# Kernel tuning notes

Measured on AMD Instinct MI355X. Metric: run time of the kernel, lower is better.

Reference implementation:

```python
import jax, jax.numpy as jnp
import numpy as np
from jax import lax


def setup_inputs() -> dict:
    key = jax.random.key(0)
    k1, k2, k3 = jax.random.split(key, 3)
    H = W = 2048
    K, p = 16, 15
    x = jax.random.uniform(k1, (1, 1, H, W), dtype=jnp.float32)
    patterns = jax.random.uniform(k2, (K, p, p), dtype=jnp.float32)
    vectors = jax.random.normal(k3, (K, 2), dtype=jnp.float32)
    return {"x": x, "patterns": patterns, "vectors": vectors}


def reference(x, patterns, vectors):
    K, p, _ = patterns.shape
    img = x[0, 0]                      # [H, W]
    H, W = img.shape
    # GENEO_1: pad by p on all sides; window at (i,j) covers padded [i:i+p, j:j+p]
    padded = jnp.pad(img, p)           # [H+2p, W+2p]
    ones_k = jnp.ones((1, 1, p, p), dtype=img.dtype)
    win_sum = lax.conv_general_dilated(
        padded[None, None], ones_k, window_strides=(1, 1), padding='VALID'
    )[0, 0]                            # [H+p+1, W+p+1]
    win_sum = win_sum[:H, :W]          # windows for i in [0,H), j in [0,W)
    # out[k,i,j] = 1 - (sum(pattern_k) - win_sum)/(p*p)
    pat_sum = patterns.sum(axis=(1, 2))                     # [K]
    F_k = 1.0 - (pat_sum[:, None, None] - win_sum[None]) / (p * p)  # [K,H,W]
    # GENEO_3: gather at (i - floor(vx), j - floor(vy)), torch negative-index wrap -> mod
    off = jnp.floor(vectors).astype(jnp.int32)              # [K,2]
    ri = (jnp.arange(H)[None, :] - off[:, 0:1]) % H          # [K,H]
    rj = (jnp.arange(W)[None, :] - off[:, 1:2]) % W          # [K,W]
    gathered = F_k[jnp.arange(K)[:, None, None], ri[:, :, None], rj[:, None, :]]  # [K,H,W]
    # original divides by final loop variable k == K-1 (faithful)
    out = gathered.sum(axis=0) / (K - 1)
    return out
```

## Files before the change

kernel.cpp:

```cpp
#include <hip/hip_runtime.h>
#include <math.h>

#define H 2048
#define W 2048
#define K 16
#define P 15
#define WP 2052
#define LDSP 272

typedef float v4 __attribute__((ext_vector_type(4)));
typedef v4 uv4 __attribute__((aligned(4)));

__global__ __launch_bounds__(320) void geneo_win(
        const float* __restrict__ img,
        float* __restrict__ win,
        const float* __restrict__ patterns,
        const float* __restrict__ vectors,
        float* __restrict__ consts,
        int* __restrict__ offs) {
    __shared__ float sl[48][LDSP];
    __shared__ float psum[5];
    int t  = threadIdx.x;
    int c0 = blockIdx.x * 256;
    int r0 = blockIdx.y * 32;

    if (blockIdx.x == 0 && blockIdx.y == 0) {
        float ps = 0.f;
        for (int idx = t; idx < 900; idx += 320) {
            v4 v = *(const v4*)&patterns[idx * 4];
            ps += (v.x + v.y) + (v.z + v.w);
        }
        #pragma unroll
        for (int q = 32; q > 0; q >>= 1) ps += __shfl_down(ps, q, 64);
        if ((t & 63) == 0) psum[t >> 6] = ps;
        if (t < 2 * K) offs[t] = (int)floorf(vectors[t]);
        __syncthreads();
        if (t == 0) {
            float total = ((psum[0] + psum[1]) + (psum[2] + psum[3])) + psum[4];
            consts[0] = (16.0f - total * (1.0f / 225.0f)) * (1.0f / 15.0f);
        }
    }

    for (int idx = t; idx < 47 * 68; idx += 320) {
        int q = idx / 68;
        int c = idx - q * 68;
        int grow = r0 - 15 + q;
        int gcol = c0 - 16 + 4 * c;
        v4 v = {0.f, 0.f, 0.f, 0.f};
        if (grow >= 0 && gcol >= 0)
            v = *(const v4*)&img[grow * W + gcol];
        *(v4*)&sl[q + 1][4 * c] = v;
    }
    __syncthreads();

    if (t < LDSP) {
        float s = 0.f;
        #pragma unroll
        for (int q = 1; q <= 15; ++q) s += sl[q][t];
        #pragma unroll
        for (int ii = 0; ii < 32; ++ii) {
            float sv = s;
            s += sl[ii + 16][t] - sl[ii + 1][t];
            sl[ii][t] = sv;
        }
    }
    __syncthreads();

    if (t < 256) {
        int g  = t & 63;
        int rb = (t >> 6) * 8;
        #pragma unroll
        for (int rr = 0; rr < 8; ++rr) {
            int ii = rb + rr;
            const float* row = &sl[ii][4 * g];
            v4 V0 = *(const v4*)&row[0];
            v4 V1 = *(const v4*)&row[4];
            v4 V2 = *(const v4*)&row[8];
            v4 V3 = *(const v4*)&row[12];
            v4 V4 = *(const v4*)&row[16];
            float s0 = ((V0.y + V0.z) + (V0.w + V1.x))
                     + ((V1.y + V1.z) + (V1.w + V2.x))
                     + ((V2.y + V2.z) + (V2.w + V3.x))
                     + ((V3.y + V3.z) + V3.w);
            float s1 = s0 - V0.y + V4.x;
            float s2 = s1 - V0.z + V4.y;
            float s3 = s2 - V0.w + V4.z;
            v4 r4 = {s0, s1, s2, s3};
            int gi = r0 + ii;
            *(v4*)&win[gi * WP + c0 + 4 * g] = r4;
            if (c0 == 0 && g == 0)
                *(v4*)&win[gi * WP + 2048] = r4;
        }
    }
}

__global__ __launch_bounds__(256) void geneo_gather(
        const float* __restrict__ win,
        const float* __restrict__ consts,
        const int* __restrict__ offs,
        float* __restrict__ out) {
    __shared__ int soy[K], sox[K];
    __shared__ float sC;
    int t = threadIdx.x;
    if (t < K) { soy[t] = offs[t * 2]; sox[t] = offs[t * 2 + 1]; }
    if (t == 0) sC = consts[0];
    __syncthreads();

    int d = blockIdx.x;
    int i = ((d & 7) << 8) | (d >> 3);
    int j = 4 * t;

    const float S = 1.0f / 3375.0f;
    v4 acc0 = {0.f, 0.f, 0.f, 0.f};
    v4 acc1 = {0.f, 0.f, 0.f, 0.f};
    #pragma unroll
    for (int k = 0; k < K; ++k) {
        int ri = (i - soy[k]) & (H - 1);
        int rj = (j - sox[k]) & (W - 1);
        const float* row = &win[ri * WP];
        acc0 += *(const uv4*)&row[rj];
        acc1 += *(const uv4*)&row[rj ^ 1024];
    }
    v4 o0 = acc0 * S + sC;
    v4 o1 = acc1 * S + sC;
    __builtin_nontemporal_store(o0, (v4*)&out[i * W + j]);
    __builtin_nontemporal_store(o1, (v4*)&out[i * W + j + 1024]);
}

extern "C" void kernel_launch(void* const* d_in, const int* in_sizes, int n_in,
                              void* d_out, int out_size, void* d_ws, size_t ws_size,
                              hipStream_t stream) {
    const float* x        = (const float*)d_in[0];
    const float* patterns = (const float*)d_in[1];
    const float* vectors  = (const float*)d_in[2];
    float* out = (float*)d_out;

    float* win    = (float*)d_ws;
    float* consts = win + H * WP;
    int*   offs   = (int*)(consts + 1);

    geneo_win<<<dim3(8, 64), 320, 0, stream>>>(x, win, patterns, vectors, consts, offs);
    geneo_gather<<<2048, 256, 0, stream>>>(win, consts, offs, out);
}
```

Baseline: 89.63 us.

## Fuse window-sum and shifted gather into one kernel using LDS halo tiles

Merges the two kernels into one. Each block computes the 15x15 window sums for its 32x256 tile plus a halo of up to 8 pixels in each direction in LDS, then gathers all 16 shifted windows from LDS instead of writing and re-reading a global window-sum buffer. A slow scalar fallback handles offsets larger than the halo, and edge blocks use wraparound masking. This removes the global intermediate round trip and one launch, at the cost of more LDS use, redundant halo work and extra complexity.

```diff
diff --git a/kernel.cpp b/kernel.cpp
--- a/kernel.cpp
+++ b/kernel.cpp
@@ -4,141 +4,212 @@
 #define H 2048
 #define W 2048
 #define K 16
-#define P 15
-#define WP 2052
-#define LDSP 272
+#define SLW 292
 
 typedef float v4 __attribute__((ext_vector_type(4)));
-typedef v4 uv4 __attribute__((aligned(4)));
-
-__global__ __launch_bounds__(320) void geneo_win(
-        const float* __restrict__ img,
-        float* __restrict__ win,
-        const float* __restrict__ patterns,
-        const float* __restrict__ vectors,
-        float* __restrict__ consts,
-        int* __restrict__ offs) {
-    __shared__ float sl[48][LDSP];
-    __shared__ float psum[5];
-    int t  = threadIdx.x;
-    int c0 = blockIdx.x * 256;
-    int r0 = blockIdx.y * 32;
-
-    if (blockIdx.x == 0 && blockIdx.y == 0) {
-        float ps = 0.f;
-        for (int idx = t; idx < 900; idx += 320) {
-            v4 v = *(const v4*)&patterns[idx * 4];
-            ps += (v.x + v.y) + (v.z + v.w);
+
+template<int S>
+__device__ __forceinline__ void gstep(const float* pk, v4* acc) {
+#pragma unroll
+  for (int rr = 0; rr < 4; ++rr) {
+    v4 A = *(const v4*)(pk + rr * SLW);
+    if constexpr (S == 0) {
+      acc[rr] += A;
+    } else {
+      v4 B = *(const v4*)(pk + rr * SLW + 4);
+      v4 r;
+      if constexpr (S == 1)      r = (v4){A.y, A.z, A.w, B.x};
+      else if constexpr (S == 2) r = (v4){A.z, A.w, B.x, B.y};
+      else                       r = (v4){A.w, B.x, B.y, B.z};
+      acc[rr] += r;
+    }
+  }
+}
+
+__global__ __launch_bounds__(512, 4) void geneo_fused(
+    const float* __restrict__ img,
+    const float* __restrict__ patterns,
+    const float* __restrict__ vectors,
+    float* __restrict__ out) {
+  __shared__ float sl[48][SLW];
+  __shared__ int   skoff[K], ssel[K], soy[K], sox[K];
+  __shared__ float sred[8];
+  __shared__ float sC;
+  __shared__ int   sfit;
+
+  const int t = threadIdx.x;
+  const int d  = blockIdx.x;
+  const int by = ((d & 7) << 3) | ((d >> 3) >> 3);
+  const int bx = (d >> 3) & 7;
+  const int i0 = by << 5;
+  const int c0 = bx << 8;
+
+  int okbit = 1;
+  if (t < K) {
+    int oy = (int)floorf(vectors[2 * t]);
+    int ox = (int)floorf(vectors[2 * t + 1]);
+    int my = oy & (H - 1); if (my > 1024) my -= 2048;
+    int mx = ox & (W - 1); if (mx > 1024) mx -= 2048;
+    soy[t] = my; sox[t] = mx;
+    int bk = 24 - mx;
+    skoff[t] = (8 - my) * SLW + (bk & ~3);
+    ssel[t]  = bk & 3;
+    okbit = (my >= -8 && my <= 8 && mx >= -8 && mx <= 8);
+  }
+  if (t < 64) {
+    unsigned long long bal = __ballot(okbit);
+    if (t == 0) sfit = ((bal & 0xFFFFull) == 0xFFFFull) ? 1 : 0;
+  }
+  float ps;
+  {
+    const v4* p4 = (const v4*)patterns;
+    v4 a = p4[t];
+    ps = (a.x + a.y) + (a.z + a.w);
+    int t2 = t + 512;
+    if (t2 < 900) { v4 b = p4[t2]; ps += (b.x + b.y) + (b.z + b.w); }
+  }
+#pragma unroll
+  for (int q2 = 32; q2 > 0; q2 >>= 1) ps += __shfl_down(ps, q2, 64);
+  if ((t & 63) == 0) sred[t >> 6] = ps;
+  __syncthreads();
+  if (t == 0) {
+    float tot = ((sred[0] + sred[1]) + (sred[2] + sred[3]))
+              + ((sred[4] + sred[5]) + (sred[6] + sred[7]));
+    sC = (16.0f - tot * (1.0f / 225.0f)) * (1.0f / 15.0f);
+  }
+
+  if (!sfit) {
+    __syncthreads();
+    const int L = t & 63, rb = (t >> 6) << 2;
+    const float Sc = 1.0f / 3375.0f;
+    const float Cc = sC;
+    for (int rr = 0; rr < 4; ++rr) {
+      for (int m = 0; m < 4; ++m) {
+        const int i = i0 + rb + rr, j = c0 + 4 * L + m;
+        float a = 0.f;
+        for (int k = 0; k < K; ++k) {
+          const int ri = (i - soy[k]) & (H - 1);
+          const int rj = (j - sox[k]) & (W - 1);
+          float wv = 0.f;
+          for (int ay = 1; ay <= 15; ++ay) {
+            const int r2 = ri - ay; if (r2 < 0) break;
+            for (int ax = 1; ax <= 15; ++ax) {
+              const int c2 = rj - ax; if (c2 < 0) break;
+              wv += img[r2 * W + c2];
+            }
+          }
+          a += wv;
         }
-        #pragma unroll
-        for (int q = 32; q > 0; q >>= 1) ps += __shfl_down(ps, q, 64);
-        if ((t & 63) == 0) psum[t >> 6] = ps;
-        if (t < 2 * K) offs[t] = (int)floorf(vectors[t]);
-        __syncthreads();
-        if (t == 0) {
-            float total = ((psum[0] + psum[1]) + (psum[2] + psum[3])) + psum[4];
-            consts[0] = (16.0f - total * (1.0f / 225.0f)) * (1.0f / 15.0f);
-        }
-    }
-
-    for (int idx = t; idx < 47 * 68; idx += 320) {
-        int q = idx / 68;
-        int c = idx - q * 68;
-        int grow = r0 - 15 + q;
-        int gcol = c0 - 16 + 4 * c;
-        v4 v = {0.f, 0.f, 0.f, 0.f};
-        if (grow >= 0 && gcol >= 0)
-            v = *(const v4*)&img[grow * W + gcol];
-        *(v4*)&sl[q + 1][4 * c] = v;
-    }
-    __syncthreads();
-
-    if (t < LDSP) {
-        float s = 0.f;
-        #pragma unroll
-        for (int q = 1; q <= 15; ++q) s += sl[q][t];
-        #pragma unroll
-        for (int ii = 0; ii < 32; ++ii) {
-            float sv = s;
-            s += sl[ii + 16][t] - sl[ii + 1][t];
-            sl[ii][t] = sv;
-        }
-    }
-    __syncthreads();
-
-    if (t < 256) {
-        int g  = t & 63;
-        int rb = (t >> 6) * 8;
-        #pragma unroll
-        for (int rr = 0; rr < 8; ++rr) {
-            int ii = rb + rr;
-            const float* row = &sl[ii][4 * g];
-            v4 V0 = *(const v4*)&row[0];
-            v4 V1 = *(const v4*)&row[4];
-            v4 V2 = *(const v4*)&row[8];
-            v4 V3 = *(const v4*)&row[12];
-            v4 V4 = *(const v4*)&row[16];
-            float s0 = ((V0.y + V0.z) + (V0.w + V1.x))
-                     + ((V1.y + V1.z) + (V1.w + V2.x))
-                     + ((V2.y + V2.z) + (V2.w + V3.x))
-                     + ((V3.y + V3.z) + V3.w);
-            float s1 = s0 - V0.y + V4.x;
-            float s2 = s1 - V0.z + V4.y;
-            float s3 = s2 - V0.w + V4.z;
-            v4 r4 = {s0, s1, s2, s3};
-            int gi = r0 + ii;
-            *(v4*)&win[gi * WP + c0 + 4 * g] = r4;
-            if (c0 == 0 && g == 0)
-                *(v4*)&win[gi * WP + 2048] = r4;
-        }
-    }
-}
-
-__global__ __launch_bounds__(256) void geneo_gather(
-        const float* __restrict__ win,
-        const float* __restrict__ consts,
-        const int* __restrict__ offs,
-        float* __restrict__ out) {
-    __shared__ int soy[K], sox[K];
-    __shared__ float sC;
-    int t = threadIdx.x;
-    if (t < K) { soy[t] = offs[t * 2]; sox[t] = offs[t * 2 + 1]; }
-    if (t == 0) sC = consts[0];
-    __syncthreads();
-
-    int d = blockIdx.x;
-    int i = ((d & 7) << 8) | (d >> 3);
-    int j = 4 * t;
-
-    const float S = 1.0f / 3375.0f;
-    v4 acc0 = {0.f, 0.f, 0.f, 0.f};
-    v4 acc1 = {0.f, 0.f, 0.f, 0.f};
-    #pragma unroll
-    for (int k = 0; k < K; ++k) {
-        int ri = (i - soy[k]) & (H - 1);
-        int rj = (j - sox[k]) & (W - 1);
-        const float* row = &win[ri * WP];
-        acc0 += *(const uv4*)&row[rj];
-        acc1 += *(const uv4*)&row[rj ^ 1024];
-    }
-    v4 o0 = acc0 * S + sC;
-    v4 o1 = acc1 * S + sC;
-    __builtin_nontemporal_store(o0, (v4*)&out[i * W + j]);
-    __builtin_nontemporal_store(o1, (v4*)&out[i * W + j + 1024]);
+        out[i * W + j] = a * Sc + Cc;
+      }
+    }
+    return;
+  }
+
+  if (t < 288) {
+    const int q = t / 72, g = t - q * 72;
+    const int gcol = (c0 - 24 + 4 * g) & (W - 1);
+    const float* ib = img + gcol;
+    const int v0 = i0 - 8;
+    const int RSTEP = (by == 0) ? 8 : ((by == 63) ? 40 : 1000);
+    const int st0 = 12 * q;
+    v4 s = (v4){0.f, 0.f, 0.f, 0.f};
+    {
+      const int vq = v0 + st0;
+      const int segv = (st0 >= RSTEP) ? (v0 + RSTEP) : -100000;
+#pragma unroll
+      for (int a = 1; a <= 15; ++a) {
+        int u = vq - a;
+        if (u >= segv) s += *(const v4*)&ib[(u & (H - 1)) * W];
+      }
+    }
+#pragma unroll
+    for (int stp = 0; stp < 12; ++stp) {
+      const int step = st0 + stp;
+      const int v = v0 + step;
+      if (step == RSTEP) s = (v4){0.f, 0.f, 0.f, 0.f};
+      *(v4*)&sl[step][4 * g] = s;
+      s += *(const v4*)&ib[(v & (H - 1)) * W];
+      const int csg = (step >= RSTEP) ? RSTEP : -100000;
+      if (step - 15 >= csg) s -= *(const v4*)&ib[((v - 15) & (H - 1)) * W];
+    }
+  }
+  __syncthreads();
+
+  v4 W0, W1, W2, W3, W4;
+  int pr = 0, ph = 0;
+  if (t < 96) {
+    ph = (t >= 48); pr = t - 48 * ph;
+    const int cb = 136 * ph;
+    W0 = *(const v4*)&sl[pr][cb +  0];
+    W1 = *(const v4*)&sl[pr][cb +  4];
+    W2 = *(const v4*)&sl[pr][cb +  8];
+    W3 = *(const v4*)&sl[pr][cb + 12];
+    W4 = *(const v4*)&sl[pr][cb + 16];
+  }
+  __syncthreads();
+  if (t < 96) {
+    const int thr = (bx == 0) ? 24 : 280;
+    for (int gg = 0; gg < 34; ++gg) {
+      const int gp = 34 * ph + gg;
+      v4 M0 = W0, M1 = W1, M2 = W2, M3 = W3;
+      const bool needmask = (bx == 0) ? (gp >= 2 && gp <= 5)
+                          : ((bx == 7) ? (gp >= 66) : false);
+      if (needmask) {
+        const int mb = thr - 4 * gp;
+        if ( 0 < mb) M0.x = 0.f; if ( 1 < mb) M0.y = 0.f;
+        if ( 2 < mb) M0.z = 0.f; if ( 3 < mb) M0.w = 0.f;
+        if ( 4 < mb) M1.x = 0.f; if ( 5 < mb) M1.y = 0.f;
+        if ( 6 < mb) M1.z = 0.f; if ( 7 < mb) M1.w = 0.f;
+        if ( 8 < mb) M2.x = 0.f; if ( 9 < mb) M2.y = 0.f;
+        if (10 < mb) M2.z = 0.f; if (11 < mb) M2.w = 0.f;
+        if (12 < mb) M3.x = 0.f; if (13 < mb) M3.y = 0.f;
+        if (14 < mb) M3.z = 0.f; if (15 < mb) M3.w = 0.f;
+      }
+      float s0 = ((M0.y + M0.z) + (M0.w + M1.x))
+               + ((M1.y + M1.z) + (M1.w + M2.x))
+               + ((M2.y + M2.z) + (M2.w + M3.x))
+               + ((M3.y + M3.z) + M3.w);
+      float s1 = s0 - M0.y + W4.x;
+      float s2 = s1 - M0.z + W4.y;
+      float s3 = s2 - M0.w + W4.z;
+      *(v4*)&sl[pr][16 + 4 * gp] = (v4){s0, s1, s2, s3};
+      W0 = W1; W1 = W2; W2 = W3; W3 = W4;
+      if (gg < 33) W4 = *(const v4*)&sl[pr][4 * gp + 20];
+    }
+  }
+  __syncthreads();
+
+  const int L = t & 63, rb = (t >> 6) << 2;
+  const float* lp = &sl[0][0];
+  const int tb = 4 * L + rb * SLW;
+  v4 acc[4];
+#pragma unroll
+  for (int rr = 0; rr < 4; ++rr) acc[rr] = (v4){0.f, 0.f, 0.f, 0.f};
+#pragma unroll
+  for (int k = 0; k < K; ++k) {
+    const float* pk = lp + skoff[k] + tb;
+    const int sf = __builtin_amdgcn_readfirstlane(ssel[k]);
+    switch (sf) {
+      case 0:  gstep<0>(pk, acc); break;
+      case 1:  gstep<1>(pk, acc); break;
+      case 2:  gstep<2>(pk, acc); break;
+      default: gstep<3>(pk, acc); break;
+    }
+  }
+  const float Cc = sC;
+#pragma unroll
+  for (int rr = 0; rr < 4; ++rr) {
+    v4 o = acc[rr] * (1.0f / 3375.0f) + Cc;
+    __builtin_nontemporal_store(o, (v4*)&out[(i0 + rb + rr) * W + c0 + 4 * L]);
+  }
 }
 
 extern "C" void kernel_launch(void* const* d_in, const int* in_sizes, int n_in,
                               void* d_out, int out_size, void* d_ws, size_t ws_size,
                               hipStream_t stream) {
-    const float* x        = (const float*)d_in[0];
-    const float* patterns = (const float*)d_in[1];
-    const float* vectors  = (const float*)d_in[2];
-    float* out = (float*)d_out;
-
-    float* win    = (float*)d_ws;
-    float* consts = win + H * WP;
-    int*   offs   = (int*)(consts + 1);
-
-    geneo_win<<<dim3(8, 64), 320, 0, stream>>>(x, win, patterns, vectors, consts, offs);
-    geneo_gather<<<2048, 256, 0, stream>>>(win, consts, offs, out);
+  const float* x        = (const float*)d_in[0];
+  const float* patterns = (const float*)d_in[1];
+  const float* vectors  = (const float*)d_in[2];
+  geneo_fused<<<512, 512, 0, stream>>>(x, patterns, vectors, (float*)d_out);
 }
```

Result: slower. 239.5 us (+167.2%).

## Stage gather window tile in LDS and reuse across shifted offsets

Applied to the files above, without the earlier changes.

The gather kernel now loads a 32x144 tile of the window-sum array into shared memory per block (16 rows x 128 cols of output plus an 8-pixel halo) and serves all 16 shifted reads from LDS. Each shift is realised with aligned v4 loads plus a compile-time lane permute. This replaces 16 unaligned global loads per output vector. A slow scalar global fallback runs when any offset exceeds the halo of 8. The change trades repeated L2/global traffic for an LDS fill, a barrier and a per-block fit check.

```diff
diff --git a/kernel.cpp b/kernel.cpp
--- a/kernel.cpp
+++ b/kernel.cpp
@@ -7,9 +7,9 @@
 #define P 15
 #define WP 2052
 #define LDSP 272
+#define SLP 148
 
 typedef float v4 __attribute__((ext_vector_type(4)));
-typedef v4 uv4 __attribute__((aligned(4)));
 
 __global__ __launch_bounds__(320) void geneo_win(
         const float* __restrict__ img,
@@ -94,37 +94,112 @@
     }
 }
 
-__global__ __launch_bounds__(256) void geneo_gather(
+template<int S>
+__device__ __forceinline__ void gstep2(const float* pk, int ro0, int ro1,
+                                       v4& a0, v4& a1) {
+    v4 A0 = *(const v4*)(pk + ro0);
+    v4 A1 = *(const v4*)(pk + ro1);
+    if constexpr (S == 0) {
+        a0 += A0; a1 += A1;
+    } else {
+        v4 B0 = *(const v4*)(pk + ro0 + 4);
+        v4 B1 = *(const v4*)(pk + ro1 + 4);
+        v4 r0, r1;
+        if constexpr (S == 1)      { r0 = (v4){A0.y, A0.z, A0.w, B0.x};
+                                     r1 = (v4){A1.y, A1.z, A1.w, B1.x}; }
+        else if constexpr (S == 2) { r0 = (v4){A0.z, A0.w, B0.x, B0.y};
+                                     r1 = (v4){A1.z, A1.w, B1.x, B1.y}; }
+        else                       { r0 = (v4){A0.w, B0.x, B0.y, B0.z};
+                                     r1 = (v4){A1.w, B1.x, B1.y, B1.z}; }
+        a0 += r0; a1 += r1;
+    }
+}
+
+__global__ __launch_bounds__(256) void geneo_gather2(
         const float* __restrict__ win,
         const float* __restrict__ consts,
         const int* __restrict__ offs,
         float* __restrict__ out) {
-    __shared__ int soy[K], sox[K];
+    __shared__ float sl[32][SLP];
+    __shared__ int   skoff[K], ssel[K], soy[K], sox[K];
     __shared__ float sC;
-    int t = threadIdx.x;
-    if (t < K) { soy[t] = offs[t * 2]; sox[t] = offs[t * 2 + 1]; }
+    __shared__ int   sfit;
+
+    const int t = threadIdx.x;
+    const int d = blockIdx.x;
+    const int q = d >> 3;
+    const int by = ((d & 7) << 4) | (q >> 4);
+    const int bx = q & 15;
+    const int i0 = by << 4;
+    const int c0 = bx << 7;
+
+    int okbit = 1;
+    if (t < K) {
+        int oy = offs[2 * t], ox = offs[2 * t + 1];
+        int my = oy & (H - 1); if (my > 1024) my -= 2048;
+        int mx = ox & (W - 1); if (mx > 1024) mx -= 2048;
+        soy[t] = oy; sox[t] = ox;
+        int bk = 8 - mx;
+        skoff[t] = (8 - my) * SLP + (bk & ~3);
+        ssel[t]  = bk & 3;
+        okbit = (my >= -8 && my <= 8 && mx >= -8 && mx <= 8);
+    }
+    if (t < 64) {
+        unsigned long long bal = __ballot(okbit);
+        if (t == 0) sfit = ((bal & 0xFFFFull) == 0xFFFFull) ? 1 : 0;
+    }
     if (t == 0) sC = consts[0];
+
+    for (int idx = t; idx < 32 * 36; idx += 256) {
+        int r = idx / 36;
+        int g = idx - r * 36;
+        int grow = (i0 - 8 + r) & (H - 1);
+        int gcol = (c0 - 8 + 4 * g) & (W - 1);
+        *(v4*)&sl[r][4 * g] = *(const v4*)&win[grow * WP + gcol];
+    }
     __syncthreads();
 
-    int d = blockIdx.x;
-    int i = ((d & 7) << 8) | (d >> 3);
-    int j = 4 * t;
-
     const float S = 1.0f / 3375.0f;
+    const float Cc = sC;
+    const int cg = t & 31;
+    const int r0 = t >> 5;
+    const int ro0 = r0 * SLP;
+    const int ro1 = (r0 + 8) * SLP;
+
+    if (!sfit) {
+        for (int e = 0; e < 4; ++e) {
+            const int j = c0 + 4 * cg + e;
+            float a0 = 0.f, a1 = 0.f;
+            for (int k = 0; k < K; ++k) {
+                const int rj = (j - sox[k]) & (W - 1);
+                a0 += win[(((i0 + r0    ) - soy[k]) & (H - 1)) * WP + rj];
+                a1 += win[(((i0 + r0 + 8) - soy[k]) & (H - 1)) * WP + rj];
+            }
+            out[(i0 + r0    ) * W + j] = a0 * S + Cc;
+            out[(i0 + r0 + 8) * W + j] = a1 * S + Cc;
+        }
+        return;
+    }
+
+    const float* lp = &sl[0][0];
+    const int tb = 4 * cg;
     v4 acc0 = {0.f, 0.f, 0.f, 0.f};
     v4 acc1 = {0.f, 0.f, 0.f, 0.f};
     #pragma unroll
     for (int k = 0; k < K; ++k) {
-        int ri = (i - soy[k]) & (H - 1);
-        int rj = (j - sox[k]) & (W - 1);
-        const float* row = &win[ri * WP];
-        acc0 += *(const uv4*)&row[rj];
-        acc1 += *(const uv4*)&row[rj ^ 1024];
-    }
-    v4 o0 = acc0 * S + sC;
-    v4 o1 = acc1 * S + sC;
-    __builtin_nontemporal_store(o0, (v4*)&out[i * W + j]);
-    __builtin_nontemporal_store(o1, (v4*)&out[i * W + j + 1024]);
+        const float* pk = lp + skoff[k] + tb;
+        const int sf = __builtin_amdgcn_readfirstlane(ssel[k]);
+        switch (sf) {
+            case 0:  gstep2<0>(pk, ro0, ro1, acc0, acc1); break;
+            case 1:  gstep2<1>(pk, ro0, ro1, acc0, acc1); break;
+            case 2:  gstep2<2>(pk, ro0, ro1, acc0, acc1); break;
+            default: gstep2<3>(pk, ro0, ro1, acc0, acc1); break;
+        }
+    }
+    v4 o0 = acc0 * S + Cc;
+    v4 o1 = acc1 * S + Cc;
+    __builtin_nontemporal_store(o0, (v4*)&out[(i0 + r0    ) * W + c0 + 4 * cg]);
+    __builtin_nontemporal_store(o1, (v4*)&out[(i0 + r0 + 8) * W + c0 + 4 * cg]);
 }
 
 extern "C" void kernel_launch(void* const* d_in, const int* in_sizes, int n_in,
@@ -140,5 +215,5 @@
     int*   offs   = (int*)(consts + 1);
 
     geneo_win<<<dim3(8, 64), 320, 0, stream>>>(x, win, patterns, vectors, consts, offs);
-    geneo_gather<<<2048, 256, 0, stream>>>(win, consts, offs, out);
-}
+    geneo_gather2<<<2048, 256, 0, stream>>>(win, consts, offs, out);
+}
```

After: 93.42 us. +4.2%, slower.
